# Kernel tuning notes

Hardware: AMD Instinct MI355X
Metric: run time of the kernel (lower is better)

The kernel has to match this reference:

```python
import jax, jax.numpy as jnp
import numpy as np

N, D_IN, D_HID, D_OUT, E = 8192, 1024, 4096, 1024, 8

def setup_inputs() -> dict:
    key = jax.random.key(0)
    ks = jax.random.split(key, 5)
    s_in = 1.0 / np.sqrt(D_IN)
    s_hid = 1.0 / np.sqrt(D_HID)
    return {
        "x": jax.random.normal(ks[0], (N, D_IN), dtype=jnp.float32),
        "W1": jax.random.normal(ks[1], (E, D_IN, D_HID), dtype=jnp.float32) * s_in,
        "b1": jnp.zeros((E, D_HID), dtype=jnp.float32),
        "W2": jax.random.normal(ks[2], (E, D_HID, D_OUT), dtype=jnp.float32) * s_hid,
        "b2": jnp.zeros((E, D_OUT), dtype=jnp.float32),
        "Wg": jax.random.normal(ks[3], (D_IN, E), dtype=jnp.float32) * s_in,
        "bg": jnp.zeros((E,), dtype=jnp.float32),
        "k": 2,
    }

def reference(x, W1, b1, W2, b2, Wg, bg, k):
    # Gating: softmax over ALL experts, then mask to top-k and renormalize
    scores = x @ Wg + bg                      # [N, E]
    _, topk_idx = jax.lax.top_k(scores, k)    # [N, k]
    mask = jax.nn.one_hot(topk_idx, scores.shape[-1], dtype=scores.dtype).sum(-2)  # [N, E]
    w = jax.nn.softmax(scores, axis=-1) * mask
    w = w / (w.sum(-1, keepdims=True) + 1e-8)  # [N, E]
    # Dense compute-all-experts (faithful to torch.stack over experts)
    h = jax.nn.relu(jnp.einsum('ni,eih->enh', x, W1) + b1[:, None, :])  # [E, N, hid]
    outs = jnp.einsum('enh,eho->eno', h, W2) + b2[:, None, :]           # [E, N, out]
    # Weighted combine over experts
    return jnp.einsum('ne,eno->no', w, outs)   # [N, out]
```

## Files before the change

### kernel.cpp

```cpp
#include <hip/hip_runtime.h>
#include <hip/hip_bf16.h>
#include <stdint.h>

#define N_TOK 8192
#define DIN   1024
#define DHID  4096
#define DOUT  1024
#define NE    8

typedef __attribute__((ext_vector_type(8))) __bf16 bf16x8;
typedef __attribute__((ext_vector_type(4))) float  f32x4;
typedef __attribute__((ext_vector_type(8))) unsigned short u16x8;

__device__ __forceinline__ unsigned short f2bfu(float f) {
    union { float f; unsigned u; } a; a.f = f;
    unsigned r = a.u + 0x7FFF + ((a.u >> 16) & 1);
    return (unsigned short)(r >> 16);
}

__device__ __forceinline__ void gload_lds16(const void* g, void* l) {
    __builtin_amdgcn_global_load_lds(
        (__attribute__((address_space(1))) void*)(void*)g,
        (__attribute__((address_space(3))) void*)l,
        16, 0, 0);
}

__device__ __forceinline__ void transpose_tile(const float* __restrict__ in,
                                               unsigned short* __restrict__ out,
                                               int R, int C, int bx, int by, int bz,
                                               float (*t)[65]) {
    const size_t RC = (size_t)R * C;
    const float* ine = in + (size_t)bz * RC;
    unsigned short* oute = out + (size_t)bz * RC;
    int c0 = bx * 64, r0 = by * 64;
    int tid = threadIdx.x;
    __syncthreads();
    #pragma unroll
    for (int it = 0; it < 4; it++) {
        int idx = it * 256 + tid;
        int r = idx >> 4, cq = (idx & 15) * 4;
        float4 v = *(const float4*)(ine + (size_t)(r0 + r) * C + c0 + cq);
        t[r][cq] = v.x; t[r][cq + 1] = v.y; t[r][cq + 2] = v.z; t[r][cq + 3] = v.w;
    }
    __syncthreads();
    #pragma unroll
    for (int it = 0; it < 2; it++) {
        int u = it * 256 + tid;
        int c = u >> 3, g = (u & 7) * 8;
        u16x8 o;
        #pragma unroll
        for (int v = 0; v < 8; v++) o[v] = f2bfu(t[g + v][c]);
        *(u16x8*)(oute + (size_t)(c0 + c) * R + r0 + g) = o;
    }
}

__global__ void gate_kernel(const float* __restrict__ x, const float* __restrict__ Wg,
                            const float* __restrict__ bg, int* __restrict__ counts,
                            int* __restrict__ tok_list, int* __restrict__ slot_list,
                            float* __restrict__ wslot, unsigned short* __restrict__ xb,
                            const float* __restrict__ W1, unsigned short* __restrict__ w1t) {
    __shared__ float tg[64][65];
    int wv = threadIdx.x >> 6, lane = threadIdx.x & 63;
    int n = blockIdx.x * 4 + wv;
    float acc[NE];
    #pragma unroll
    for (int e = 0; e < NE; e++) acc[e] = 0.f;
    const float* xr = x + (size_t)n * DIN;
    unsigned short* xbr = xb + (size_t)n * DIN;
    #pragma unroll
    for (int i = 0; i < DIN / 256; i++) {
        int d = i * 256 + lane * 4;
        float4 xv = *(const float4*)(xr + d);
        ushort4 o;
        o.x = f2bfu(xv.x); o.y = f2bfu(xv.y); o.z = f2bfu(xv.z); o.w = f2bfu(xv.w);
        *(ushort4*)(xbr + d) = o;
        const float* w = Wg + (size_t)d * NE;
        #pragma unroll
        for (int u = 0; u < 4; u++) {
            float xs = (&xv.x)[u];
            float4 w0 = *(const float4*)(w + u * NE);
            float4 w1 = *(const float4*)(w + u * NE + 4);
            acc[0] += xs * w0.x; acc[1] += xs * w0.y; acc[2] += xs * w0.z; acc[3] += xs * w0.w;
            acc[4] += xs * w1.x; acc[5] += xs * w1.y; acc[6] += xs * w1.z; acc[7] += xs * w1.w;
        }
    }
    #pragma unroll
    for (int off = 32; off; off >>= 1)
        #pragma unroll
        for (int e = 0; e < NE; e++) acc[e] += __shfl_down(acc[e], off);
    if (lane == 0) {
        float s[NE], p[NE];
        float mx = -1e30f;
        #pragma unroll
        for (int e = 0; e < NE; e++) { s[e] = acc[e] + bg[e]; mx = fmaxf(mx, s[e]); }
        float sum = 0.f;
        #pragma unroll
        for (int e = 0; e < NE; e++) { p[e] = expf(s[e] - mx); sum += p[e]; }
        float inv = 1.f / sum;
        int e0 = 0;
        #pragma unroll
        for (int e = 1; e < NE; e++) if (s[e] > s[e0]) e0 = e;
        int e1 = (e0 == 0) ? 1 : 0;
        #pragma unroll
        for (int e = 0; e < NE; e++) if (e != e0 && s[e] > s[e1]) e1 = e;
        float p0 = p[e0] * inv, p1 = p[e1] * inv;
        float rn = 1.f / (p0 + p1 + 1e-8f);
        int pos0 = atomicAdd(&counts[e0], 1);
        tok_list[e0 * N_TOK + pos0] = n; slot_list[e0 * N_TOK + pos0] = 2 * n;     wslot[e0 * N_TOK + pos0] = p0 * rn;
        int pos1 = atomicAdd(&counts[e1], 1);
        tok_list[e1 * N_TOK + pos1] = n; slot_list[e1 * N_TOK + pos1] = 2 * n + 1; wslot[e1 * N_TOK + pos1] = p1 * rn;
    }
    #pragma unroll 1
    for (int j = 0; j < 4; j++) {
        int id = blockIdx.x * 4 + j;
        int bx = id & 63, by = (id >> 6) & 15, bz = id >> 10;
        transpose_tile(W1, w1t, DIN, DHID, bx, by, bz, tg);
    }
}

template <int KDIM, int NDIM, bool IS_GEMM1, int SPLITK>
__global__ __launch_bounds__(256, 4)
void moe_gemm(const unsigned short* __restrict__ Asrc, const unsigned short* __restrict__ Bt,
              const float* __restrict__ bias, unsigned short* __restrict__ Hdst,
              float* __restrict__ Odst, const int* __restrict__ counts,
              const int* __restrict__ tok_list, const int* __restrict__ slot_list,
              const float* __restrict__ wslot,
              const float* __restrict__ W2src, unsigned short* __restrict__ w2t_dst) {
    constexpr int NT_N = NDIM / 128;
    constexpr int NT_M = N_TOK / 128;
    constexpr int KLEN = KDIM / SPLITK;

    int e = blockIdx.x & 7;
    int local = blockIdx.x >> 3;
    int count = counts[e];

    __shared__ __align__(16) unsigned short pool[2 * 128 * 64];
    unsigned short* As = pool;
    unsigned short* Bs = pool + 128 * 64;
    __shared__ int rowid_s[128];
    __shared__ int outid_s[128];
    __shared__ float w_s[128];

    int tid = threadIdx.x;
    int lane = tid & 63;
    int wv = tid >> 6;
    int ric = lane >> 3;
    int k8  = (lane & 7) ^ ric;
    int wm = (wv >> 1) * 64, wn = (wv & 1) * 64;
    int r16 = lane & 15, quad = lane >> 4;

    bool tdone = !IS_GEMM1;

    for (int w = local; ; w += 128) {
        int tile_n = w % NT_N;
        int r = w / NT_N;
        int kh = r % SPLITK;
        int tile_m = r / SPLITK;
        if (tile_m >= NT_M) break;
        if (tile_m * 128 >= count) break;

        __syncthreads();
        if (tid < 128) {
            int rr = tile_m * 128 + tid;
            if (rr >= count) rr = tile_m * 128;
            int base = e * N_TOK + rr;
            if (IS_GEMM1) { rowid_s[tid] = tok_list[base]; outid_s[tid] = slot_list[base]; }
            else          { rowid_s[tid] = slot_list[base]; outid_s[tid] = tok_list[base]; w_s[tid] = wslot[base]; }
        }
        __syncthreads();

        const int k0 = kh * KLEN;
        const unsigned short* aptr[4];
        const unsigned short* bptr[4];
        #pragma unroll
        for (int i = 0; i < 4; i++) {
            int c = wv * 4 + i;
            int row = c * 8 + ric;
            aptr[i] = Asrc + (size_t)rowid_s[row] * KDIM + k0 + k8 * 8;
            bptr[i] = Bt + ((size_t)e * NDIM + tile_n * 128 + row) * KDIM + k0 + k8 * 8;
        }

        f32x4 acc[4][4];
        #pragma unroll
        for (int i = 0; i < 4; i++)
            #pragma unroll
            for (int j = 0; j < 4; j++) acc[i][j] = (f32x4){0.f, 0.f, 0.f, 0.f};

        for (int kk = 0; kk < KLEN / 64; kk++) {
            #pragma unroll
            for (int i = 0; i < 4; i++) {
                gload_lds16(aptr[i] + kk * 64, (void*)(As + (wv * 4 + i) * 512));
                gload_lds16(bptr[i] + kk * 64, (void*)(Bs + (wv * 4 + i) * 512));
            }
            __syncthreads();
            #pragma unroll
            for (int kh2 = 0; kh2 < 2; kh2++) {
                int swk = ((kh2 * 4 + quad) ^ (r16 & 7)) * 8;
                bf16x8 av[4], bv[4];
                #pragma unroll
                for (int i = 0; i < 4; i++)
                    av[i] = *(const bf16x8*)(As + (wm + i * 16 + r16) * 64 + swk);
                #pragma unroll
                for (int j = 0; j < 4; j++)
                    bv[j] = *(const bf16x8*)(Bs + (wn + j * 16 + r16) * 64 + swk);
                #pragma unroll
                for (int i = 0; i < 4; i++)
                    #pragma unroll
                    for (int j = 0; j < 4; j++)
                        acc[i][j] = __builtin_amdgcn_mfma_f32_16x16x32_bf16(av[i], bv[j], acc[i][j], 0, 0, 0);
            }
            __syncthreads();
        }

        float bias_r[4];
        #pragma unroll
        for (int j = 0; j < 4; j++)
            bias_r[j] = bias[(size_t)e * NDIM + tile_n * 128 + wn + j * 16 + r16];
        #pragma unroll
        for (int i = 0; i < 4; i++) {
            #pragma unroll
            for (int reg = 0; reg < 4; reg++) {
                int rr = wm + i * 16 + quad * 4 + reg;
                if (tile_m * 128 + rr >= count) continue;
                #pragma unroll
                for (int j = 0; j < 4; j++) {
                    int col = tile_n * 128 + wn + j * 16 + r16;
                    float v = acc[i][j][reg];
                    if (IS_GEMM1) {
                        v = fmaxf(v + bias_r[j], 0.f);
                        Hdst[(size_t)outid_s[rr] * NDIM + col] = f2bfu(v);
                    } else {
                        if (kh == 0) v += bias_r[j];
                        atomicAdd(&Odst[(size_t)outid_s[rr] * NDIM + col], w_s[rr] * v);
                    }
                }
            }
        }

        if constexpr (IS_GEMM1) {
            if (!tdone) {
                tdone = true;
                float (*t)[65] = (float(*)[65])pool;
                #pragma unroll 1
                for (int j = 0; j < 8; j++) {
                    int id = blockIdx.x * 8 + j;
                    int bx = id & 15, by = (id >> 4) & 63, bz = id >> 10;
                    transpose_tile(W2src, w2t_dst, DHID, DOUT, bx, by, bz, t);
                }
            }
        }
    }

    if constexpr (IS_GEMM1) {
        if (!tdone) {
            float (*t)[65] = (float(*)[65])pool;
            #pragma unroll 1
            for (int j = 0; j < 8; j++) {
                int id = blockIdx.x * 8 + j;
                int bx = id & 15, by = (id >> 4) & 63, bz = id >> 10;
                transpose_tile(W2src, w2t_dst, DHID, DOUT, bx, by, bz, t);
            }
        }
    }
}

extern "C" void kernel_launch(void* const* d_in, const int* in_sizes, int n_in,
                              void* d_out, int out_size, void* d_ws, size_t ws_size,
                              hipStream_t stream) {
    const float* x  = (const float*)d_in[0];
    const float* W1 = (const float*)d_in[1];
    const float* b1 = (const float*)d_in[2];
    const float* W2 = (const float*)d_in[3];
    const float* b2 = (const float*)d_in[4];
    const float* Wg = (const float*)d_in[5];
    const float* bg = (const float*)d_in[6];
    float* out = (float*)d_out;

    char* ws = (char*)d_ws;
    unsigned short* xb  = (unsigned short*)(ws + 0);
    unsigned short* w1t = (unsigned short*)(ws + 16777216);
    unsigned short* w2t = (unsigned short*)(ws + 83886080);
    unsigned short* h   = (unsigned short*)(ws + 150994944);
    int*   counts    = (int*)(ws + 285212672);
    int*   tok_list  = (int*)(ws + 285212928);
    int*   slot_list = (int*)(ws + 285475072);
    float* wslot     = (float*)(ws + 285737216);

    hipMemsetAsync(counts, 0, 256, stream);
    hipMemsetAsync(d_out, 0, (size_t)out_size * sizeof(float), stream);

    gate_kernel<<<N_TOK / 4, 256, 0, stream>>>(x, Wg, bg, counts, tok_list, slot_list, wslot, xb,
                                               W1, w1t);

    moe_gemm<DIN, DHID, true, 1><<<1024, 256, 0, stream>>>(
        xb, w1t, b1, h, nullptr, counts, tok_list, slot_list, wslot, W2, w2t);
    moe_gemm<DHID, DOUT, false, 2><<<1024, 256, 0, stream>>>(
        h, w2t, b2, nullptr, out, counts, tok_list, slot_list, wslot, nullptr, nullptr);
}
```

Baseline: 843.9 us.

## Use 256-row tiles for GEMM1, stage H stores through LDS, fuse output zeroing

GEMM1 now uses a 256x128 tile with 768 persistent blocks, so each B tile is reused across more rows and less operand traffic is needed per FLOP. Its epilogue writes the bf16 results into per-wave LDS scratch and then issues 16-byte row stores, replacing scattered 2-byte global writes. The output memset is folded into the gate kernel, and the W2 transpose work is redistributed across fewer blocks. The larger tile raises register and LDS use, which lowers occupancy to 3 blocks per CU.

```diff
diff --git a/kernel.cpp b/kernel.cpp
--- a/kernel.cpp
+++ b/kernel.cpp
@@ -58,7 +58,8 @@
                             const float* __restrict__ bg, int* __restrict__ counts,
                             int* __restrict__ tok_list, int* __restrict__ slot_list,
                             float* __restrict__ wslot, unsigned short* __restrict__ xb,
-                            const float* __restrict__ W1, unsigned short* __restrict__ w1t) {
+                            const float* __restrict__ W1, unsigned short* __restrict__ w1t,
+                            float* __restrict__ out_zero) {
     __shared__ float tg[64][65];
     int wv = threadIdx.x >> 6, lane = threadIdx.x & 63;
     int n = blockIdx.x * 4 + wv;
@@ -110,6 +111,12 @@
         int pos1 = atomicAdd(&counts[e1], 1);
         tok_list[e1 * N_TOK + pos1] = n; slot_list[e1 * N_TOK + pos1] = 2 * n + 1; wslot[e1 * N_TOK + pos1] = p1 * rn;
     }
+    {
+        float4 z = {0.f, 0.f, 0.f, 0.f};
+        float* ob = out_zero + ((size_t)blockIdx.x * 256 + threadIdx.x) * 16;
+        #pragma unroll
+        for (int j = 0; j < 4; j++) *(float4*)(ob + j * 4) = z;
+    }
     #pragma unroll 1
     for (int j = 0; j < 4; j++) {
         int id = blockIdx.x * 4 + j;
@@ -118,8 +125,8 @@
     }
 }
 
-template <int KDIM, int NDIM, bool IS_GEMM1, int SPLITK>
-__global__ __launch_bounds__(256, 4)
+template <int BM, int KDIM, int NDIM, bool IS_GEMM1, int SPLITK, int NBLK>
+__global__ __launch_bounds__(256, (BM == 256) ? 3 : 4)
 void moe_gemm(const unsigned short* __restrict__ Asrc, const unsigned short* __restrict__ Bt,
               const float* __restrict__ bias, unsigned short* __restrict__ Hdst,
               float* __restrict__ Odst, const int* __restrict__ counts,
@@ -127,84 +134,90 @@
               const float* __restrict__ wslot,
               const float* __restrict__ W2src, unsigned short* __restrict__ w2t_dst) {
     constexpr int NT_N = NDIM / 128;
-    constexpr int NT_M = N_TOK / 128;
+    constexpr int NT_M = N_TOK / BM;
     constexpr int KLEN = KDIM / SPLITK;
+    constexpr int MFR  = BM / 32;
+    constexpr int NA   = BM / 32;
 
     int e = blockIdx.x & 7;
     int local = blockIdx.x >> 3;
     int count = counts[e];
 
-    __shared__ __align__(16) unsigned short pool[2 * 128 * 64];
+    __shared__ __align__(16) unsigned short pool[(BM + 128) * 64];
     unsigned short* As = pool;
-    unsigned short* Bs = pool + 128 * 64;
-    __shared__ int rowid_s[128];
-    __shared__ int outid_s[128];
-    __shared__ float w_s[128];
+    unsigned short* Bs = pool + BM * 64;
+    __shared__ int rowid_s[BM];
+    __shared__ int outid_s[BM];
+    __shared__ float w_s[BM];
 
     int tid = threadIdx.x;
     int lane = tid & 63;
     int wv = tid >> 6;
     int ric = lane >> 3;
     int k8  = (lane & 7) ^ ric;
-    int wm = (wv >> 1) * 64, wn = (wv & 1) * 64;
+    int wm = (wv >> 1) * (BM / 2), wn = (wv & 1) * 64;
     int r16 = lane & 15, quad = lane >> 4;
 
     bool tdone = !IS_GEMM1;
 
-    for (int w = local; ; w += 128) {
+    for (int w = local; ; w += NBLK) {
         int tile_n = w % NT_N;
         int r = w / NT_N;
         int kh = r % SPLITK;
         int tile_m = r / SPLITK;
         if (tile_m >= NT_M) break;
-        if (tile_m * 128 >= count) break;
+        if (tile_m * BM >= count) break;
 
         __syncthreads();
-        if (tid < 128) {
-            int rr = tile_m * 128 + tid;
-            if (rr >= count) rr = tile_m * 128;
+        for (int t0 = tid; t0 < BM; t0 += 256) {
+            int rr = tile_m * BM + t0;
+            if (rr >= count) rr = tile_m * BM;
             int base = e * N_TOK + rr;
-            if (IS_GEMM1) { rowid_s[tid] = tok_list[base]; outid_s[tid] = slot_list[base]; }
-            else          { rowid_s[tid] = slot_list[base]; outid_s[tid] = tok_list[base]; w_s[tid] = wslot[base]; }
+            if (IS_GEMM1) { rowid_s[t0] = tok_list[base]; outid_s[t0] = slot_list[base]; }
+            else          { rowid_s[t0] = slot_list[base]; outid_s[t0] = tok_list[base]; w_s[t0] = wslot[base]; }
         }
         __syncthreads();
 
         const int k0 = kh * KLEN;
-        const unsigned short* aptr[4];
+        const unsigned short* aptr[NA];
         const unsigned short* bptr[4];
+        #pragma unroll
+        for (int i = 0; i < NA; i++) {
+            int c = wv * NA + i;
+            aptr[i] = Asrc + (size_t)rowid_s[c * 8 + ric] * KDIM + k0 + k8 * 8;
+        }
         #pragma unroll
         for (int i = 0; i < 4; i++) {
             int c = wv * 4 + i;
-            int row = c * 8 + ric;
-            aptr[i] = Asrc + (size_t)rowid_s[row] * KDIM + k0 + k8 * 8;
-            bptr[i] = Bt + ((size_t)e * NDIM + tile_n * 128 + row) * KDIM + k0 + k8 * 8;
-        }
-
-        f32x4 acc[4][4];
-        #pragma unroll
-        for (int i = 0; i < 4; i++)
+            bptr[i] = Bt + ((size_t)e * NDIM + tile_n * 128 + c * 8 + ric) * KDIM + k0 + k8 * 8;
+        }
+
+        f32x4 acc[MFR][4];
+        #pragma unroll
+        for (int i = 0; i < MFR; i++)
             #pragma unroll
             for (int j = 0; j < 4; j++) acc[i][j] = (f32x4){0.f, 0.f, 0.f, 0.f};
 
         for (int kk = 0; kk < KLEN / 64; kk++) {
             #pragma unroll
-            for (int i = 0; i < 4; i++) {
-                gload_lds16(aptr[i] + kk * 64, (void*)(As + (wv * 4 + i) * 512));
+            for (int i = 0; i < NA; i++)
+                gload_lds16(aptr[i] + kk * 64, (void*)(As + (wv * NA + i) * 512));
+            #pragma unroll
+            for (int i = 0; i < 4; i++)
                 gload_lds16(bptr[i] + kk * 64, (void*)(Bs + (wv * 4 + i) * 512));
-            }
             __syncthreads();
             #pragma unroll
             for (int kh2 = 0; kh2 < 2; kh2++) {
                 int swk = ((kh2 * 4 + quad) ^ (r16 & 7)) * 8;
-                bf16x8 av[4], bv[4];
-                #pragma unroll
-                for (int i = 0; i < 4; i++)
+                bf16x8 av[MFR], bv[4];
+                #pragma unroll
+                for (int i = 0; i < MFR; i++)
                     av[i] = *(const bf16x8*)(As + (wm + i * 16 + r16) * 64 + swk);
                 #pragma unroll
                 for (int j = 0; j < 4; j++)
                     bv[j] = *(const bf16x8*)(Bs + (wn + j * 16 + r16) * 64 + swk);
                 #pragma unroll
-                for (int i = 0; i < 4; i++)
+                for (int i = 0; i < MFR; i++)
                     #pragma unroll
                     for (int j = 0; j < 4; j++)
                         acc[i][j] = __builtin_amdgcn_mfma_f32_16x16x32_bf16(av[i], bv[j], acc[i][j], 0, 0, 0);
@@ -216,20 +229,48 @@
         #pragma unroll
         for (int j = 0; j < 4; j++)
             bias_r[j] = bias[(size_t)e * NDIM + tile_n * 128 + wn + j * 16 + r16];
-        #pragma unroll
-        for (int i = 0; i < 4; i++) {
-            #pragma unroll
-            for (int reg = 0; reg < 4; reg++) {
-                int rr = wm + i * 16 + quad * 4 + reg;
-                if (tile_m * 128 + rr >= count) continue;
-                #pragma unroll
-                for (int j = 0; j < 4; j++) {
-                    int col = tile_n * 128 + wn + j * 16 + r16;
-                    float v = acc[i][j][reg];
-                    if (IS_GEMM1) {
-                        v = fmaxf(v + bias_r[j], 0.f);
-                        Hdst[(size_t)outid_s[rr] * NDIM + col] = f2bfu(v);
-                    } else {
+
+        if constexpr (IS_GEMM1) {
+            char* sl = (char*)pool + wv * 12288;
+            #pragma unroll
+            for (int ch = 0; ch < MFR / 4; ch++) {
+                #pragma unroll
+                for (int fi = 0; fi < 4; fi++) {
+                    int f = ch * 4 + fi;
+                    #pragma unroll
+                    for (int reg = 0; reg < 4; reg++) {
+                        int rl = fi * 16 + quad * 4 + reg;
+                        #pragma unroll
+                        for (int j = 0; j < 4; j++) {
+                            int col = j * 16 + r16;
+                            float v = fmaxf(acc[f][j][reg] + bias_r[j], 0.f);
+                            *(unsigned short*)(sl + rl * 144 + col * 2) = f2bfu(v);
+                        }
+                    }
+                }
+                asm volatile("s_waitcnt lgkmcnt(0)" ::: "memory");
+                int rgrp = lane >> 3, s8 = lane & 7;
+                #pragma unroll
+                for (int it = 0; it < 8; it++) {
+                    int rl = it * 8 + rgrp;
+                    int rr = wm + ch * 64 + rl;
+                    u16x8 vv = *(const u16x8*)(sl + rl * 144 + s8 * 16);
+                    if (tile_m * BM + rr < count)
+                        *(u16x8*)(Hdst + (size_t)outid_s[rr] * NDIM + tile_n * 128 + wn + s8 * 8) = vv;
+                }
+                asm volatile("s_waitcnt lgkmcnt(0)" ::: "memory");
+            }
+        } else {
+            #pragma unroll
+            for (int i = 0; i < MFR; i++) {
+                #pragma unroll
+                for (int reg = 0; reg < 4; reg++) {
+                    int rr = wm + i * 16 + quad * 4 + reg;
+                    if (tile_m * BM + rr >= count) continue;
+                    #pragma unroll
+                    for (int j = 0; j < 4; j++) {
+                        int col = tile_n * 128 + wn + j * 16 + r16;
+                        float v = acc[i][j][reg];
                         if (kh == 0) v += bias_r[j];
                         atomicAdd(&Odst[(size_t)outid_s[rr] * NDIM + col], w_s[rr] * v);
                     }
@@ -242,8 +283,9 @@
                 tdone = true;
                 float (*t)[65] = (float(*)[65])pool;
                 #pragma unroll 1
-                for (int j = 0; j < 8; j++) {
-                    int id = blockIdx.x * 8 + j;
+                for (int j = 0; j < 11; j++) {
+                    int id = blockIdx.x * 11 + j;
+                    if (id >= 8192) break;
                     int bx = id & 15, by = (id >> 4) & 63, bz = id >> 10;
                     transpose_tile(W2src, w2t_dst, DHID, DOUT, bx, by, bz, t);
                 }
@@ -255,8 +297,9 @@
         if (!tdone) {
             float (*t)[65] = (float(*)[65])pool;
             #pragma unroll 1
-            for (int j = 0; j < 8; j++) {
-                int id = blockIdx.x * 8 + j;
+            for (int j = 0; j < 11; j++) {
+                int id = blockIdx.x * 11 + j;
+                if (id >= 8192) break;
                 int bx = id & 15, by = (id >> 4) & 63, bz = id >> 10;
                 transpose_tile(W2src, w2t_dst, DHID, DOUT, bx, by, bz, t);
             }
@@ -287,13 +330,12 @@
     float* wslot     = (float*)(ws + 285737216);
 
     hipMemsetAsync(counts, 0, 256, stream);
-    hipMemsetAsync(d_out, 0, (size_t)out_size * sizeof(float), stream);
 
     gate_kernel<<<N_TOK / 4, 256, 0, stream>>>(x, Wg, bg, counts, tok_list, slot_list, wslot, xb,
-                                               W1, w1t);
-
-    moe_gemm<DIN, DHID, true, 1><<<1024, 256, 0, stream>>>(
+                                               W1, w1t, out);
+
+    moe_gemm<256, DIN, DHID, true, 1, 96><<<768, 256, 0, stream>>>(
         xb, w1t, b1, h, nullptr, counts, tok_list, slot_list, wslot, W2, w2t);
-    moe_gemm<DHID, DOUT, false, 2><<<1024, 256, 0, stream>>>(
+    moe_gemm<128, DHID, DOUT, false, 2, 128><<<1024, 256, 0, stream>>>(
         h, w2t, b2, nullptr, out, counts, tok_list, slot_list, wslot, nullptr, nullptr);
 }
```

New measurement: 965.4 us. 14.4% more time.

## Use atomic work-stealing tile scheduler across experts and fuse output zeroing into gate

Applied to the files above, without the earlier changes.

Replaces the static per-expert tile assignment (each block bound to one expert, striding by 128) with a dynamic scheduler. A per-expert atomic cursor lets blocks claim tiles from their own expert first and steal from other experts once it is exhausted. This targets load imbalance caused by uneven expert token counts. It also zeroes the output buffer inside the gate kernel instead of through a separate memset. In exchange, each tile now costs an atomic plus an extra barrier, and tile ordering changes from tile_m-major to tile_n-major, which can affect cache reuse.

```diff
diff --git a/kernel.cpp b/kernel.cpp
--- a/kernel.cpp
+++ b/kernel.cpp
@@ -58,7 +58,8 @@
                             const float* __restrict__ bg, int* __restrict__ counts,
                             int* __restrict__ tok_list, int* __restrict__ slot_list,
                             float* __restrict__ wslot, unsigned short* __restrict__ xb,
-                            const float* __restrict__ W1, unsigned short* __restrict__ w1t) {
+                            const float* __restrict__ W1, unsigned short* __restrict__ w1t,
+                            float* __restrict__ out_zero) {
     __shared__ float tg[64][65];
     int wv = threadIdx.x >> 6, lane = threadIdx.x & 63;
     int n = blockIdx.x * 4 + wv;
@@ -110,6 +111,12 @@
         int pos1 = atomicAdd(&counts[e1], 1);
         tok_list[e1 * N_TOK + pos1] = n; slot_list[e1 * N_TOK + pos1] = 2 * n + 1; wslot[e1 * N_TOK + pos1] = p1 * rn;
     }
+    {
+        float4 z = {0.f, 0.f, 0.f, 0.f};
+        float* ob = out_zero + ((size_t)blockIdx.x * 256 + threadIdx.x) * 16;
+        #pragma unroll
+        for (int j = 0; j < 4; j++) *(float4*)(ob + j * 4) = z;
+    }
     #pragma unroll 1
     for (int j = 0; j < 4; j++) {
         int id = blockIdx.x * 4 + j;
@@ -124,15 +131,12 @@
               const float* __restrict__ bias, unsigned short* __restrict__ Hdst,
               float* __restrict__ Odst, const int* __restrict__ counts,
               const int* __restrict__ tok_list, const int* __restrict__ slot_list,
-              const float* __restrict__ wslot,
+              const float* __restrict__ wslot, int* __restrict__ cursor,
               const float* __restrict__ W2src, unsigned short* __restrict__ w2t_dst) {
     constexpr int NT_N = NDIM / 128;
-    constexpr int NT_M = N_TOK / 128;
     constexpr int KLEN = KDIM / SPLITK;
 
-    int e = blockIdx.x & 7;
-    int local = blockIdx.x >> 3;
-    int count = counts[e];
+    int e_own = blockIdx.x & 7;
 
     __shared__ __align__(16) unsigned short pool[2 * 128 * 64];
     unsigned short* As = pool;
@@ -140,6 +144,7 @@
     __shared__ int rowid_s[128];
     __shared__ int outid_s[128];
     __shared__ float w_s[128];
+    __shared__ int meta_s[5];
 
     int tid = threadIdx.x;
     int lane = tid & 63;
@@ -150,16 +155,39 @@
     int r16 = lane & 15, quad = lane >> 4;
 
     bool tdone = !IS_GEMM1;
-
-    for (int w = local; ; w += 128) {
-        int tile_n = w % NT_N;
-        int r = w / NT_N;
-        int kh = r % SPLITK;
-        int tile_m = r / SPLITK;
-        if (tile_m >= NT_M) break;
-        if (tile_m * 128 >= count) break;
-
+    unsigned dmask = 0;
+
+    for (;;) {
         __syncthreads();
+        if (tid == 0) {
+            int sel_e = -1, sel_idx = 0;
+            #pragma unroll 1
+            for (int t = 0; t < 8 && sel_e < 0; t++) {
+                int ee = (e_own + t) & 7;
+                if (dmask & (1u << ee)) continue;
+                int p = atomicAdd(&cursor[ee], 1);
+                int cnte = counts[ee];
+                int Mte = (cnte + 127) >> 7;
+                if (p < Mte * NT_N * SPLITK) { sel_e = ee; sel_idx = p; }
+                else dmask |= (1u << ee);
+            }
+            if (sel_e < 0) meta_s[0] = -1;
+            else {
+                int cnte = counts[sel_e];
+                int Mte = (cnte + 127) >> 7;
+                int MS = Mte * SPLITK;
+                int tn = sel_idx / MS;
+                int rem = sel_idx - tn * MS;
+                int tm = rem % Mte;
+                int kh = rem / Mte;
+                meta_s[0] = sel_e; meta_s[1] = tn; meta_s[2] = kh; meta_s[3] = tm; meta_s[4] = cnte;
+            }
+        }
+        __syncthreads();
+        int e = meta_s[0];
+        if (e < 0) break;
+        int tile_n = meta_s[1], kh = meta_s[2], tile_m = meta_s[3], count = meta_s[4];
+
         if (tid < 128) {
             int rr = tile_m * 128 + tid;
             if (rr >= count) rr = tile_m * 128;
@@ -282,18 +310,19 @@
     unsigned short* w2t = (unsigned short*)(ws + 83886080);
     unsigned short* h   = (unsigned short*)(ws + 150994944);
     int*   counts    = (int*)(ws + 285212672);
+    int*   cur1      = counts + 8;
+    int*   cur2      = counts + 16;
     int*   tok_list  = (int*)(ws + 285212928);
     int*   slot_list = (int*)(ws + 285475072);
     float* wslot     = (float*)(ws + 285737216);
 
     hipMemsetAsync(counts, 0, 256, stream);
-    hipMemsetAsync(d_out, 0, (size_t)out_size * sizeof(float), stream);
 
     gate_kernel<<<N_TOK / 4, 256, 0, stream>>>(x, Wg, bg, counts, tok_list, slot_list, wslot, xb,
-                                               W1, w1t);
+                                               W1, w1t, out);
 
     moe_gemm<DIN, DHID, true, 1><<<1024, 256, 0, stream>>>(
-        xb, w1t, b1, h, nullptr, counts, tok_list, slot_list, wslot, W2, w2t);
+        xb, w1t, b1, h, nullptr, counts, tok_list, slot_list, wslot, cur1, W2, w2t);
     moe_gemm<DHID, DOUT, false, 2><<<1024, 256, 0, stream>>>(
-        h, w2t, b2, nullptr, out, counts, tok_list, slot_list, wslot, nullptr, nullptr);
-}
+        h, w2t, b2, nullptr, out, counts, tok_list, slot_list, wslot, cur2, nullptr, nullptr);
+}
```

Result: slower. 1.171 ms (+38.7%).
